# Kernel tuning notes

Measured on AMD Instinct MI355X. Metric: run time of the kernel, lower is better.

The kernel has to match this reference:

```python
import jax, jax.numpy as jnp
import numpy as np

SEQ, B, IN, H, OUT = 600, 4096, 6, 30, 61


def setup_inputs() -> dict:
    key = jax.random.key(0)
    ks = jax.random.split(key, 9)
    s_ih = 1.0 / np.sqrt(H)
    return {
        "X": jax.random.normal(ks[0], (SEQ, B, IN), dtype=jnp.float32),
        "W_ih": jax.random.uniform(ks[1], (4 * H, IN), jnp.float32, -s_ih, s_ih),
        "W_hh": jax.random.uniform(ks[2], (4 * H, H), jnp.float32, -s_ih, s_ih),
        "b_ih": jax.random.uniform(ks[3], (4 * H,), jnp.float32, -s_ih, s_ih),
        "b_hh": jax.random.uniform(ks[4], (4 * H,), jnp.float32, -s_ih, s_ih),
        "W1": jax.random.uniform(ks[5], (H, H), jnp.float32, -s_ih, s_ih),
        "b1": jax.random.uniform(ks[6], (H,), jnp.float32, -s_ih, s_ih),
        "W2": jax.random.uniform(ks[7], (OUT, H), jnp.float32, -s_ih, s_ih),
        "b2": jax.random.uniform(ks[8], (OUT,), jnp.float32, -s_ih, s_ih),
        "batch_size": B,
    }


def _lstm_last_h(X, W_ih, W_hh, b_ih, b_hh):
    # Precompute input projections for all timesteps: [T, B, 4H]
    xg = jnp.einsum("tbi,gi->tbg", X, W_ih) + b_ih + b_hh
    h0 = jnp.zeros((X.shape[1], W_hh.shape[1]), X.dtype)
    c0 = jnp.zeros_like(h0)

    def step(carry, xg_t):
        h, c = carry
        g = xg_t + h @ W_hh.T  # [B, 4H]
        i, f, gg, o = jnp.split(g, 4, axis=-1)  # PyTorch gate order i,f,g,o
        c = jax.nn.sigmoid(f) * c + jax.nn.sigmoid(i) * jnp.tanh(gg)
        h = jax.nn.sigmoid(o) * jnp.tanh(c)
        return (h, c), None

    (h, _), _ = jax.lax.scan(step, (h0, c0), xg)
    return h  # out[-1, :, :]


def reference(X, W_ih, W_hh, b_ih, b_hh, W1, b1, W2, b2, batch_size):
    h = _lstm_last_h(X, W_ih, W_hh, b_ih, b_hh)
    out = h @ W1.T + b1  # fc1
    # dropout(p=0.6) is identity in eval mode
    out = out @ W2.T + b2  # fc2
    return out  # [B, 61]
```

## Files before the change

kernel.cpp:

```cpp
#include <hip/hip_runtime.h>


#define SEQ   600
#define BATCH 4096
#define INP   6
#define HID   30
#define NOUT  61
#define EPB   8

__device__ __forceinline__ float rcp_(float x) { return __builtin_amdgcn_rcpf(x); }
__device__ __forceinline__ float sigm_(float x) { return rcp_(1.0f + __expf(-x)); }
__device__ __forceinline__ float tanh_(float x) {
    float e = __expf(2.0f * x);
    return 1.0f - 2.0f * rcp_(e + 1.0f);
}

extern "C" __global__ void __launch_bounds__(256, 2)
lstm_fused(const float* __restrict__ X,   const float* __restrict__ Wih,
           const float* __restrict__ Whh, const float* __restrict__ bih,
           const float* __restrict__ bhh, const float* __restrict__ W1,
           const float* __restrict__ b1,  const float* __restrict__ W2,
           const float* __restrict__ b2,  float* __restrict__ out)
{
    __shared__ float h_sh[EPB][32];
    __shared__ float o1_sh[EPB][32];

    const int tid  = threadIdx.x;
    const int u    = tid & 31;
    const int e    = tid >> 5;
    const int b    = blockIdx.x * EPB + e;
    const bool act = (u < HID);

    h_sh[e][u] = 0.0f;

    float wi[32], wf[32], wg[32], wo[32];
    float vi[INP], vf[INP], vg[INP], vo[INP];
    float bi = 0.f, bf = 0.f, bg = 0.f, bo = 0.f;
    #pragma unroll
    for (int k = 0; k < 32; ++k) { wi[k] = 0.f; wf[k] = 0.f; wg[k] = 0.f; wo[k] = 0.f; }
    #pragma unroll
    for (int k = 0; k < INP; ++k) { vi[k] = 0.f; vf[k] = 0.f; vg[k] = 0.f; vo[k] = 0.f; }

    if (act) {
        #pragma unroll
        for (int k = 0; k < HID; ++k) {
            wi[k] = Whh[(0 * HID + u) * HID + k];
            wf[k] = Whh[(1 * HID + u) * HID + k];
            wg[k] = Whh[(2 * HID + u) * HID + k];
            wo[k] = Whh[(3 * HID + u) * HID + k];
        }
        #pragma unroll
        for (int k = 0; k < INP; ++k) {
            vi[k] = Wih[(0 * HID + u) * INP + k];
            vf[k] = Wih[(1 * HID + u) * INP + k];
            vg[k] = Wih[(2 * HID + u) * INP + k];
            vo[k] = Wih[(3 * HID + u) * INP + k];
        }
        bi = bih[0 * HID + u] + bhh[0 * HID + u];
        bf = bih[1 * HID + u] + bhh[1 * HID + u];
        bg = bih[2 * HID + u] + bhh[2 * HID + u];
        bo = bih[3 * HID + u] + bhh[3 * HID + u];
    }

    float c = 0.f, h = 0.f;
    float x[INP], xn[INP] = {};
    {
        const float* p = X + (size_t)b * INP;
        #pragma unroll
        for (int k = 0; k < INP; ++k) x[k] = p[k];
    }
    asm volatile("s_waitcnt lgkmcnt(0)" ::: "memory");

    const float4* h4p = (const float4*)(&h_sh[e][0]);

    for (int t = 0; t < SEQ; ++t) {
        if (t + 1 < SEQ) {
            const float* p = X + ((size_t)(t + 1) * BATCH + b) * INP;
            #pragma unroll
            for (int k = 0; k < INP; ++k) xn[k] = p[k];
        }

        float ai = bi, af = bf, ag = bg, ao = bo;
        #pragma unroll
        for (int k = 0; k < INP; ++k) {
            ai = fmaf(vi[k], x[k], ai);
            af = fmaf(vf[k], x[k], af);
            ag = fmaf(vg[k], x[k], ag);
            ao = fmaf(vo[k], x[k], ao);
        }
        #pragma unroll
        for (int q = 0; q < 8; ++q) {
            float4 hv = h4p[q];
            ai = fmaf(wi[4*q+0], hv.x, ai); af = fmaf(wf[4*q+0], hv.x, af);
            ag = fmaf(wg[4*q+0], hv.x, ag); ao = fmaf(wo[4*q+0], hv.x, ao);
            ai = fmaf(wi[4*q+1], hv.y, ai); af = fmaf(wf[4*q+1], hv.y, af);
            ag = fmaf(wg[4*q+1], hv.y, ag); ao = fmaf(wo[4*q+1], hv.y, ao);
            ai = fmaf(wi[4*q+2], hv.z, ai); af = fmaf(wf[4*q+2], hv.z, af);
            ag = fmaf(wg[4*q+2], hv.z, ag); ao = fmaf(wo[4*q+2], hv.z, ao);
            ai = fmaf(wi[4*q+3], hv.w, ai); af = fmaf(wf[4*q+3], hv.w, af);
            ag = fmaf(wg[4*q+3], hv.w, ag); ao = fmaf(wo[4*q+3], hv.w, ao);
        }

        float gi = sigm_(ai);
        float gf = sigm_(af);
        float go = sigm_(ao);
        float gg = tanh_(ag);
        c = gf * c + gi * gg;
        h = go * tanh_(c);

        h_sh[e][u] = h;
        asm volatile("s_waitcnt lgkmcnt(0)" ::: "memory");

        #pragma unroll
        for (int k = 0; k < INP; ++k) x[k] = xn[k];
    }

    if (act) {
        float a1 = b1[u];
        const float* w1r = W1 + u * HID;
        #pragma unroll
        for (int k = 0; k < HID; ++k) a1 = fmaf(w1r[k], h_sh[e][k], a1);
        o1_sh[e][u] = a1;
    }
    asm volatile("s_waitcnt lgkmcnt(0)" ::: "memory");

    if (act) {
        for (int o = u; o < NOUT; o += HID) {
            float a2 = b2[o];
            const float* w2r = W2 + o * HID;
            #pragma unroll
            for (int k = 0; k < HID; ++k) a2 = fmaf(w2r[k], o1_sh[e][k], a2);
            out[(size_t)b * NOUT + o] = a2;
        }
    }
}

extern "C" void kernel_launch(void* const* d_in, const int* in_sizes, int n_in,
                              void* d_out, int out_size, void* d_ws, size_t ws_size,
                              hipStream_t stream) {
    const float* X   = (const float*)d_in[0];
    const float* Wih = (const float*)d_in[1];
    const float* Whh = (const float*)d_in[2];
    const float* bih = (const float*)d_in[3];
    const float* bhh = (const float*)d_in[4];
    const float* W1  = (const float*)d_in[5];
    const float* b1  = (const float*)d_in[6];
    const float* W2  = (const float*)d_in[7];
    const float* b2  = (const float*)d_in[8];
    float* out = (float*)d_out;

    dim3 grid(BATCH / EPB);
    dim3 block(256);
    hipLaunchKernelGGL(lstm_fused, grid, block, 0, stream,
                       X, Wih, Whh, bih, bhh, W1, b1, W2, b2, out);
}
```

Before: 360.3 us.

## Rewrite LSTM recurrence as inline-asm loop with fp16 dot2 and packed weights

Rewrites the recurrent loop as one hand-written inline-assembly block. Weights and the hidden state are packed into fp16 pairs so v_dot2_f32_f16 does two MACs per instruction, and h is stored in LDS as fp16. Blocks shrink to one 64-lane wavefront holding two batch elements, and X loads are software-prefetched one step ahead. This aims to cut VALU instruction count and LDS traffic on the serial critical path. In exchange it lowers precision of weights, inputs and hidden state over 600 steps, which risks accuracy drift, and the hand-placed waitcnt/nop scheduling risks hazards.

```diff
diff --git a/kernel.cpp b/kernel.cpp
--- a/kernel.cpp
+++ b/kernel.cpp
@@ -6,131 +6,274 @@
 #define INP   6
 #define HID   30
 #define NOUT  61
-#define EPB   8
-
-__device__ __forceinline__ float rcp_(float x) { return __builtin_amdgcn_rcpf(x); }
-__device__ __forceinline__ float sigm_(float x) { return rcp_(1.0f + __expf(-x)); }
-__device__ __forceinline__ float tanh_(float x) {
-    float e = __expf(2.0f * x);
-    return 1.0f - 2.0f * rcp_(e + 1.0f);
+
+typedef __fp16 f16;
+typedef f16 f16x2 __attribute__((ext_vector_type(2)));
+typedef unsigned u32;
+typedef __attribute__((address_space(3))) f16 lds_f16;
+
+__device__ __forceinline__ u32 cvtpk(float a, float b) {
+    union { f16x2 h; u32 u; } c;
+    c.h = __builtin_amdgcn_cvt_pkrtz(a, b);
+    return c.u;
 }
 
-extern "C" __global__ void __launch_bounds__(256, 2)
-lstm_fused(const float* __restrict__ X,   const float* __restrict__ Wih,
-           const float* __restrict__ Whh, const float* __restrict__ bih,
-           const float* __restrict__ bhh, const float* __restrict__ W1,
-           const float* __restrict__ b1,  const float* __restrict__ W2,
-           const float* __restrict__ b2,  float* __restrict__ out)
+extern "C" __global__ void __launch_bounds__(64, 2)
+lstm_asm(const float* __restrict__ X,   const float* __restrict__ Wih,
+         const float* __restrict__ Whh, const float* __restrict__ bih,
+         const float* __restrict__ bhh, const float* __restrict__ W1,
+         const float* __restrict__ b1,  const float* __restrict__ W2,
+         const float* __restrict__ b2,  float* __restrict__ out)
 {
-    __shared__ float h_sh[EPB][32];
-    __shared__ float o1_sh[EPB][32];
-
-    const int tid  = threadIdx.x;
-    const int u    = tid & 31;
-    const int e    = tid >> 5;
-    const int b    = blockIdx.x * EPB + e;
+    __shared__ __align__(8) f16 h_sh[2][32];
+    __shared__ __align__(8) f16 trash[64];
+    __shared__ float o1_sh[2][32];
+
+    const int lane = threadIdx.x;
+    const int half = lane >> 5;
+    const int u    = lane & 31;
+    const int uu   = (u < HID) ? u : (HID - 1);
+    const int b    = blockIdx.x * 2 + half;
     const bool act = (u < HID);
 
-    h_sh[e][u] = 0.0f;
-
-    float wi[32], wf[32], wg[32], wo[32];
-    float vi[INP], vf[INP], vg[INP], vo[INP];
-    float bi = 0.f, bf = 0.f, bg = 0.f, bo = 0.f;
+    h_sh[half][u] = (f16)0.f;
+
+    u32 W[60], XW[12];
     #pragma unroll
-    for (int k = 0; k < 32; ++k) { wi[k] = 0.f; wf[k] = 0.f; wg[k] = 0.f; wo[k] = 0.f; }
-    #pragma unroll
-    for (int k = 0; k < INP; ++k) { vi[k] = 0.f; vf[k] = 0.f; vg[k] = 0.f; vo[k] = 0.f; }
+    for (int g = 0; g < 4; ++g) {
+        const float* r = Whh + (g * HID + uu) * HID;
+        #pragma unroll
+        for (int j = 0; j < 15; ++j) W[g * 15 + j] = cvtpk(r[2 * j], r[2 * j + 1]);
+        const float* s = Wih + (g * HID + uu) * INP;
+        #pragma unroll
+        for (int j = 0; j < 3; ++j) XW[g * 3 + j] = cvtpk(s[2 * j], s[2 * j + 1]);
+    }
+    const float B0 = bih[0 * HID + uu] + bhh[0 * HID + uu];
+    const float B1 = bih[1 * HID + uu] + bhh[1 * HID + uu];
+    const float B2 = bih[2 * HID + uu] + bhh[2 * HID + uu];
+    const float B3 = bih[3 * HID + uu] + bhh[3 * HID + uu];
+    const float NL = -1.4426950408889634f;
+    const float L2 = 2.8853900817779268f;
+
+    const unsigned ha = (unsigned)(unsigned long long)(lds_f16*)&h_sh[half][0];
+    const unsigned wa = act
+        ? (unsigned)(unsigned long long)(lds_f16*)&h_sh[half][u]
+        : (unsigned)(unsigned long long)(lds_f16*)&trash[lane];
+
+    float x0 = X[(size_t)b * INP + 0], x1 = X[(size_t)b * INP + 1];
+    float x2 = X[(size_t)b * INP + 2], x3 = X[(size_t)b * INP + 3];
+    float x4 = X[(size_t)b * INP + 4], x5 = X[(size_t)b * INP + 5];
+    const float* xbase = X + (size_t)blockIdx.x * 2 * INP;
+    unsigned vo = (unsigned)(BATCH * INP * 4) + (unsigned)(half * INP * 4);
+
+    float a0=0,a1=0,a2=0,a3=0,a4=0,a5=0,a6=0,a7=0;
+    float t0=0,t1=0,t2=0,t3=0,t4=0,t5=0,t6=0,t7=0;
+    u32 h0=0,h1=0,h2=0,h3=0,h4=0,h5=0,h6=0,h7=0,h8=0,h9=0,h10=0,h11=0,h12=0,h13=0,h14=0;
+    u32 p0=0,p1=0,p2=0,hh=0;
+    float c=0.f;
+    unsigned cnt = SEQ, st2 = 0;
+    const unsigned stride = BATCH * INP * 4;
+
+    asm volatile(
+        "9:\n\t"
+        "s_waitcnt vmcnt(0)\n\t"
+        "v_cvt_pkrtz_f16_f32 %[p0], %[x0], %[x1]\n\t"
+        "v_cvt_pkrtz_f16_f32 %[p1], %[x2], %[x3]\n\t"
+        "v_cvt_pkrtz_f16_f32 %[p2], %[x4], %[x5]\n\t"
+        "global_load_dword %[x0], %[vo], %[xb] offset:0\n\t"
+        "global_load_dword %[x1], %[vo], %[xb] offset:4\n\t"
+        "global_load_dword %[x2], %[vo], %[xb] offset:8\n\t"
+        "global_load_dword %[x3], %[vo], %[xb] offset:12\n\t"
+        "global_load_dword %[x4], %[vo], %[xb] offset:16\n\t"
+        "global_load_dword %[x5], %[vo], %[xb] offset:20\n\t"
+        "s_cmp_ge_u32 %[cnt], 3\n\t"
+        "s_cselect_b32 %[st2], %[st], 0\n\t"
+        "v_add_u32 %[vo], %[st2], %[vo]\n\t"
+        "ds_read_b32 %[h0],  %[ha] offset:0\n\t"
+        "ds_read_b32 %[h1],  %[ha] offset:4\n\t"
+        "ds_read_b32 %[h2],  %[ha] offset:8\n\t"
+        "ds_read_b32 %[h3],  %[ha] offset:12\n\t"
+        "ds_read_b32 %[h4],  %[ha] offset:16\n\t"
+        "ds_read_b32 %[h5],  %[ha] offset:20\n\t"
+        "ds_read_b32 %[h6],  %[ha] offset:24\n\t"
+        "ds_read_b32 %[h7],  %[ha] offset:28\n\t"
+        "ds_read_b32 %[h8],  %[ha] offset:32\n\t"
+        "ds_read_b32 %[h9],  %[ha] offset:36\n\t"
+        "ds_read_b32 %[h10], %[ha] offset:40\n\t"
+        "ds_read_b32 %[h11], %[ha] offset:44\n\t"
+        "ds_read_b32 %[h12], %[ha] offset:48\n\t"
+        "ds_read_b32 %[h13], %[ha] offset:52\n\t"
+        "ds_read_b32 %[h14], %[ha] offset:56\n\t"
+        "v_mov_b32 %[a0], %[bi0]\n\t"
+        "v_mov_b32 %[a1], %[bi1]\n\t"
+        "v_mov_b32 %[a2], %[bi2]\n\t"
+        "v_mov_b32 %[a3], %[bi3]\n\t"
+        "v_mov_b32 %[a4], 0\n\t"
+        "v_mov_b32 %[a5], 0\n\t"
+        "v_mov_b32 %[a6], 0\n\t"
+        "v_mov_b32 %[a7], 0\n\t"
+        "s_waitcnt lgkmcnt(0)\n\t"
+        "v_dot2_f32_f16 %[a0], %[w0],  %[h0],  %[a0]\n\t"
+        "v_dot2_f32_f16 %[a1], %[w15], %[h0],  %[a1]\n\t"
+        "v_dot2_f32_f16 %[a2], %[w30], %[h0],  %[a2]\n\t"
+        "v_dot2_f32_f16 %[a3], %[w45], %[h0],  %[a3]\n\t"
+        "v_dot2_f32_f16 %[a4], %[w1],  %[h1],  %[a4]\n\t"
+        "v_dot2_f32_f16 %[a5], %[w16], %[h1],  %[a5]\n\t"
+        "v_dot2_f32_f16 %[a6], %[w31], %[h1],  %[a6]\n\t"
+        "v_dot2_f32_f16 %[a7], %[w46], %[h1],  %[a7]\n\t"
+        "v_dot2_f32_f16 %[a0], %[w2],  %[h2],  %[a0]\n\t"
+        "v_dot2_f32_f16 %[a1], %[w17], %[h2],  %[a1]\n\t"
+        "v_dot2_f32_f16 %[a2], %[w32], %[h2],  %[a2]\n\t"
+        "v_dot2_f32_f16 %[a3], %[w47], %[h2],  %[a3]\n\t"
+        "v_dot2_f32_f16 %[a4], %[w3],  %[h3],  %[a4]\n\t"
+        "v_dot2_f32_f16 %[a5], %[w18], %[h3],  %[a5]\n\t"
+        "v_dot2_f32_f16 %[a6], %[w33], %[h3],  %[a6]\n\t"
+        "v_dot2_f32_f16 %[a7], %[w48], %[h3],  %[a7]\n\t"
+        "v_dot2_f32_f16 %[a0], %[w4],  %[h4],  %[a0]\n\t"
+        "v_dot2_f32_f16 %[a1], %[w19], %[h4],  %[a1]\n\t"
+        "v_dot2_f32_f16 %[a2], %[w34], %[h4],  %[a2]\n\t"
+        "v_dot2_f32_f16 %[a3], %[w49], %[h4],  %[a3]\n\t"
+        "v_dot2_f32_f16 %[a4], %[w5],  %[h5],  %[a4]\n\t"
+        "v_dot2_f32_f16 %[a5], %[w20], %[h5],  %[a5]\n\t"
+        "v_dot2_f32_f16 %[a6], %[w35], %[h5],  %[a6]\n\t"
+        "v_dot2_f32_f16 %[a7], %[w50], %[h5],  %[a7]\n\t"
+        "v_dot2_f32_f16 %[a0], %[w6],  %[h6],  %[a0]\n\t"
+        "v_dot2_f32_f16 %[a1], %[w21], %[h6],  %[a1]\n\t"
+        "v_dot2_f32_f16 %[a2], %[w36], %[h6],  %[a2]\n\t"
+        "v_dot2_f32_f16 %[a3], %[w51], %[h6],  %[a3]\n\t"
+        "v_dot2_f32_f16 %[a4], %[w7],  %[h7],  %[a4]\n\t"
+        "v_dot2_f32_f16 %[a5], %[w22], %[h7],  %[a5]\n\t"
+        "v_dot2_f32_f16 %[a6], %[w37], %[h7],  %[a6]\n\t"
+        "v_dot2_f32_f16 %[a7], %[w52], %[h7],  %[a7]\n\t"
+        "v_dot2_f32_f16 %[a0], %[w8],  %[h8],  %[a0]\n\t"
+        "v_dot2_f32_f16 %[a1], %[w23], %[h8],  %[a1]\n\t"
+        "v_dot2_f32_f16 %[a2], %[w38], %[h8],  %[a2]\n\t"
+        "v_dot2_f32_f16 %[a3], %[w53], %[h8],  %[a3]\n\t"
+        "v_dot2_f32_f16 %[a4], %[w9],  %[h9],  %[a4]\n\t"
+        "v_dot2_f32_f16 %[a5], %[w24], %[h9],  %[a5]\n\t"
+        "v_dot2_f32_f16 %[a6], %[w39], %[h9],  %[a6]\n\t"
+        "v_dot2_f32_f16 %[a7], %[w54], %[h9],  %[a7]\n\t"
+        "v_dot2_f32_f16 %[a0], %[w10], %[h10], %[a0]\n\t"
+        "v_dot2_f32_f16 %[a1], %[w25], %[h10], %[a1]\n\t"
+        "v_dot2_f32_f16 %[a2], %[w40], %[h10], %[a2]\n\t"
+        "v_dot2_f32_f16 %[a3], %[w55], %[h10], %[a3]\n\t"
+        "v_dot2_f32_f16 %[a4], %[w11], %[h11], %[a4]\n\t"
+        "v_dot2_f32_f16 %[a5], %[w26], %[h11], %[a5]\n\t"
+        "v_dot2_f32_f16 %[a6], %[w41], %[h11], %[a6]\n\t"
+        "v_dot2_f32_f16 %[a7], %[w56], %[h11], %[a7]\n\t"
+        "v_dot2_f32_f16 %[a0], %[w12], %[h12], %[a0]\n\t"
+        "v_dot2_f32_f16 %[a1], %[w27], %[h12], %[a1]\n\t"
+        "v_dot2_f32_f16 %[a2], %[w42], %[h12], %[a2]\n\t"
+        "v_dot2_f32_f16 %[a3], %[w57], %[h12], %[a3]\n\t"
+        "v_dot2_f32_f16 %[a4], %[w13], %[h13], %[a4]\n\t"
+        "v_dot2_f32_f16 %[a5], %[w28], %[h13], %[a5]\n\t"
+        "v_dot2_f32_f16 %[a6], %[w43], %[h13], %[a6]\n\t"
+        "v_dot2_f32_f16 %[a7], %[w58], %[h13], %[a7]\n\t"
+        "v_dot2_f32_f16 %[a0], %[w14], %[h14], %[a0]\n\t"
+        "v_dot2_f32_f16 %[a1], %[w29], %[h14], %[a1]\n\t"
+        "v_dot2_f32_f16 %[a2], %[w44], %[h14], %[a2]\n\t"
+        "v_dot2_f32_f16 %[a3], %[w59], %[h14], %[a3]\n\t"
+        "v_dot2_f32_f16 %[a4], %[xw0],  %[p0], %[a4]\n\t"
+        "v_dot2_f32_f16 %[a5], %[xw3],  %[p0], %[a5]\n\t"
+        "v_dot2_f32_f16 %[a6], %[xw6],  %[p0], %[a6]\n\t"
+        "v_dot2_f32_f16 %[a7], %[xw9],  %[p0], %[a7]\n\t"
+        "v_dot2_f32_f16 %[a0], %[xw1],  %[p1], %[a0]\n\t"
+        "v_dot2_f32_f16 %[a1], %[xw4],  %[p1], %[a1]\n\t"
+        "v_dot2_f32_f16 %[a2], %[xw7],  %[p1], %[a2]\n\t"
+        "v_dot2_f32_f16 %[a3], %[xw10], %[p1], %[a3]\n\t"
+        "v_dot2_f32_f16 %[a4], %[xw2],  %[p2], %[a4]\n\t"
+        "v_dot2_f32_f16 %[a5], %[xw5],  %[p2], %[a5]\n\t"
+        "v_dot2_f32_f16 %[a6], %[xw8],  %[p2], %[a6]\n\t"
+        "v_dot2_f32_f16 %[a7], %[xw11], %[p2], %[a7]\n\t"
+        "v_add_f32 %[a0], %[a0], %[a4]\n\t"
+        "v_add_f32 %[a1], %[a1], %[a5]\n\t"
+        "v_add_f32 %[a2], %[a2], %[a6]\n\t"
+        "v_add_f32 %[a3], %[a3], %[a7]\n\t"
+        "v_mul_f32 %[t0], %[nl], %[a0]\n\t"
+        "v_mul_f32 %[t1], %[nl], %[a1]\n\t"
+        "v_mul_f32 %[t2], %[l2], %[a2]\n\t"
+        "v_mul_f32 %[t3], %[nl], %[a3]\n\t"
+        "v_exp_f32 %[t0], %[t0]\n\t"
+        "v_exp_f32 %[t1], %[t1]\n\t"
+        "v_exp_f32 %[t2], %[t2]\n\t"
+        "v_exp_f32 %[t3], %[t3]\n\t"
+        "v_add_f32 %[t0], 1.0, %[t0]\n\t"
+        "v_add_f32 %[t1], 1.0, %[t1]\n\t"
+        "v_add_f32 %[t2], 1.0, %[t2]\n\t"
+        "v_add_f32 %[t3], 1.0, %[t3]\n\t"
+        "v_rcp_f32 %[t0], %[t0]\n\t"
+        "v_rcp_f32 %[t1], %[t1]\n\t"
+        "v_rcp_f32 %[t2], %[t2]\n\t"
+        "v_rcp_f32 %[t3], %[t3]\n\t"
+        "v_add_f32 %[t4], %[t2], %[t2]\n\t"
+        "v_sub_f32 %[t2], 1.0, %[t4]\n\t"
+        "v_mul_f32 %[t5], %[t0], %[t2]\n\t"
+        "v_fma_f32 %[c], %[t1], %[c], %[t5]\n\t"
+        "v_mul_f32 %[t6], %[l2], %[c]\n\t"
+        "v_exp_f32 %[t6], %[t6]\n\t"
+        "s_nop 0\n\t"
+        "v_add_f32 %[t6], 1.0, %[t6]\n\t"
+        "v_rcp_f32 %[t6], %[t6]\n\t"
+        "s_nop 0\n\t"
+        "v_add_f32 %[t7], %[t6], %[t6]\n\t"
+        "v_sub_f32 %[t6], 1.0, %[t7]\n\t"
+        "v_mul_f32 %[t7], %[t3], %[t6]\n\t"
+        "v_cvt_f16_f32 %[hh], %[t7]\n\t"
+        "ds_write_b16 %[wa], %[hh]\n\t"
+        "s_sub_u32 %[cnt], %[cnt], 1\n\t"
+        "s_cmp_lg_u32 %[cnt], 0\n\t"
+        "s_cbranch_scc1 9b\n\t"
+        "s_waitcnt vmcnt(0) lgkmcnt(0)\n\t"
+        : [a0]"+v"(a0),[a1]"+v"(a1),[a2]"+v"(a2),[a3]"+v"(a3),
+          [a4]"+v"(a4),[a5]"+v"(a5),[a6]"+v"(a6),[a7]"+v"(a7),
+          [t0]"+v"(t0),[t1]"+v"(t1),[t2]"+v"(t2),[t3]"+v"(t3),
+          [t4]"+v"(t4),[t5]"+v"(t5),[t6]"+v"(t6),[t7]"+v"(t7),
+          [h0]"+v"(h0),[h1]"+v"(h1),[h2]"+v"(h2),[h3]"+v"(h3),
+          [h4]"+v"(h4),[h5]"+v"(h5),[h6]"+v"(h6),[h7]"+v"(h7),
+          [h8]"+v"(h8),[h9]"+v"(h9),[h10]"+v"(h10),[h11]"+v"(h11),
+          [h12]"+v"(h12),[h13]"+v"(h13),[h14]"+v"(h14),
+          [p0]"+v"(p0),[p1]"+v"(p1),[p2]"+v"(p2),[hh]"+v"(hh),
+          [c]"+v"(c),
+          [x0]"+v"(x0),[x1]"+v"(x1),[x2]"+v"(x2),
+          [x3]"+v"(x3),[x4]"+v"(x4),[x5]"+v"(x5),
+          [vo]"+v"(vo),[cnt]"+s"(cnt),[st2]"+s"(st2)
+        : [w0]"v"(W[0]),[w1]"v"(W[1]),[w2]"v"(W[2]),[w3]"v"(W[3]),[w4]"v"(W[4]),
+          [w5]"v"(W[5]),[w6]"v"(W[6]),[w7]"v"(W[7]),[w8]"v"(W[8]),[w9]"v"(W[9]),
+          [w10]"v"(W[10]),[w11]"v"(W[11]),[w12]"v"(W[12]),[w13]"v"(W[13]),[w14]"v"(W[14]),
+          [w15]"v"(W[15]),[w16]"v"(W[16]),[w17]"v"(W[17]),[w18]"v"(W[18]),[w19]"v"(W[19]),
+          [w20]"v"(W[20]),[w21]"v"(W[21]),[w22]"v"(W[22]),[w23]"v"(W[23]),[w24]"v"(W[24]),
+          [w25]"v"(W[25]),[w26]"v"(W[26]),[w27]"v"(W[27]),[w28]"v"(W[28]),[w29]"v"(W[29]),
+          [w30]"v"(W[30]),[w31]"v"(W[31]),[w32]"v"(W[32]),[w33]"v"(W[33]),[w34]"v"(W[34]),
+          [w35]"v"(W[35]),[w36]"v"(W[36]),[w37]"v"(W[37]),[w38]"v"(W[38]),[w39]"v"(W[39]),
+          [w40]"v"(W[40]),[w41]"v"(W[41]),[w42]"v"(W[42]),[w43]"v"(W[43]),[w44]"v"(W[44]),
+          [w45]"v"(W[45]),[w46]"v"(W[46]),[w47]"v"(W[47]),[w48]"v"(W[48]),[w49]"v"(W[49]),
+          [w50]"v"(W[50]),[w51]"v"(W[51]),[w52]"v"(W[52]),[w53]"v"(W[53]),[w54]"v"(W[54]),
+          [w55]"v"(W[55]),[w56]"v"(W[56]),[w57]"v"(W[57]),[w58]"v"(W[58]),[w59]"v"(W[59]),
+          [xw0]"v"(XW[0]),[xw1]"v"(XW[1]),[xw2]"v"(XW[2]),[xw3]"v"(XW[3]),
+          [xw4]"v"(XW[4]),[xw5]"v"(XW[5]),[xw6]"v"(XW[6]),[xw7]"v"(XW[7]),
+          [xw8]"v"(XW[8]),[xw9]"v"(XW[9]),[xw10]"v"(XW[10]),[xw11]"v"(XW[11]),
+          [bi0]"v"(B0),[bi1]"v"(B1),[bi2]"v"(B2),[bi3]"v"(B3),
+          [nl]"v"(NL),[l2]"v"(L2),
+          [ha]"v"(ha),[wa]"v"(wa),
+          [xb]"s"(xbase),[st]"s"(stride)
+        : "vcc","scc","memory");
 
     if (act) {
+        float a1v = b1[u];
+        const float* w1r = W1 + u * HID;
         #pragma unroll
-        for (int k = 0; k < HID; ++k) {
-            wi[k] = Whh[(0 * HID + u) * HID + k];
-            wf[k] = Whh[(1 * HID + u) * HID + k];
-            wg[k] = Whh[(2 * HID + u) * HID + k];
-            wo[k] = Whh[(3 * HID + u) * HID + k];
-        }
-        #pragma unroll
-        for (int k = 0; k < INP; ++k) {
-            vi[k] = Wih[(0 * HID + u) * INP + k];
-            vf[k] = Wih[(1 * HID + u) * INP + k];
-            vg[k] = Wih[(2 * HID + u) * INP + k];
-            vo[k] = Wih[(3 * HID + u) * INP + k];
-        }
-        bi = bih[0 * HID + u] + bhh[0 * HID + u];
-        bf = bih[1 * HID + u] + bhh[1 * HID + u];
-        bg = bih[2 * HID + u] + bhh[2 * HID + u];
-        bo = bih[3 * HID + u] + bhh[3 * HID + u];
-    }
-
-    float c = 0.f, h = 0.f;
-    float x[INP], xn[INP] = {};
-    {
-        const float* p = X + (size_t)b * INP;
-        #pragma unroll
-        for (int k = 0; k < INP; ++k) x[k] = p[k];
+        for (int k = 0; k < HID; ++k) a1v = fmaf(w1r[k], (float)h_sh[half][k], a1v);
+        o1_sh[half][u] = a1v;
     }
     asm volatile("s_waitcnt lgkmcnt(0)" ::: "memory");
 
-    const float4* h4p = (const float4*)(&h_sh[e][0]);
-
-    for (int t = 0; t < SEQ; ++t) {
-        if (t + 1 < SEQ) {
-            const float* p = X + ((size_t)(t + 1) * BATCH + b) * INP;
-            #pragma unroll
-            for (int k = 0; k < INP; ++k) xn[k] = p[k];
-        }
-
-        float ai = bi, af = bf, ag = bg, ao = bo;
-        #pragma unroll
-        for (int k = 0; k < INP; ++k) {
-            ai = fmaf(vi[k], x[k], ai);
-            af = fmaf(vf[k], x[k], af);
-            ag = fmaf(vg[k], x[k], ag);
-            ao = fmaf(vo[k], x[k], ao);
-        }
-        #pragma unroll
-        for (int q = 0; q < 8; ++q) {
-            float4 hv = h4p[q];
-            ai = fmaf(wi[4*q+0], hv.x, ai); af = fmaf(wf[4*q+0], hv.x, af);
-            ag = fmaf(wg[4*q+0], hv.x, ag); ao = fmaf(wo[4*q+0], hv.x, ao);
-            ai = fmaf(wi[4*q+1], hv.y, ai); af = fmaf(wf[4*q+1], hv.y, af);
-            ag = fmaf(wg[4*q+1], hv.y, ag); ao = fmaf(wo[4*q+1], hv.y, ao);
-            ai = fmaf(wi[4*q+2], hv.z, ai); af = fmaf(wf[4*q+2], hv.z, af);
-            ag = fmaf(wg[4*q+2], hv.z, ag); ao = fmaf(wo[4*q+2], hv.z, ao);
-            ai = fmaf(wi[4*q+3], hv.w, ai); af = fmaf(wf[4*q+3], hv.w, af);
-            ag = fmaf(wg[4*q+3], hv.w, ag); ao = fmaf(wo[4*q+3], hv.w, ao);
-        }
-
-        float gi = sigm_(ai);
-        float gf = sigm_(af);
-        float go = sigm_(ao);
-        float gg = tanh_(ag);
-        c = gf * c + gi * gg;
-        h = go * tanh_(c);
-
-        h_sh[e][u] = h;
-        asm volatile("s_waitcnt lgkmcnt(0)" ::: "memory");
-
-        #pragma unroll
-        for (int k = 0; k < INP; ++k) x[k] = xn[k];
-    }
-
-    if (act) {
-        float a1 = b1[u];
-        const float* w1r = W1 + u * HID;
-        #pragma unroll
-        for (int k = 0; k < HID; ++k) a1 = fmaf(w1r[k], h_sh[e][k], a1);
-        o1_sh[e][u] = a1;
-    }
-    asm volatile("s_waitcnt lgkmcnt(0)" ::: "memory");
-
     if (act) {
         for (int o = u; o < NOUT; o += HID) {
-            float a2 = b2[o];
+            float a2v = b2[o];
             const float* w2r = W2 + o * HID;
             #pragma unroll
-            for (int k = 0; k < HID; ++k) a2 = fmaf(w2r[k], o1_sh[e][k], a2);
-            out[(size_t)b * NOUT + o] = a2;
+            for (int k = 0; k < HID; ++k) a2v = fmaf(w2r[k], o1_sh[half][k], a2v);
+            out[(size_t)b * NOUT + o] = a2v;
         }
     }
 }
@@ -149,8 +292,8 @@
     const float* b2  = (const float*)d_in[8];
     float* out = (float*)d_out;
 
-    dim3 grid(BATCH / EPB);
-    dim3 block(256);
-    hipLaunchKernelGGL(lstm_fused, grid, block, 0, stream,
+    dim3 grid(BATCH / 2);
+    dim3 block(64);
+    hipLaunchKernelGGL(lstm_asm, grid, block, 0, stream,
                        X, Wih, Whh, bih, bhh, W1, b1, W2, b2, out);
 }
```

Result: faster. 323.9 us (-10.1%).
